# Kernel tuning notes

Hardware: AMD Instinct MI355X
Metric: run time of the kernel (lower is better)

Reference implementation:

```python
import jax, jax.numpy as jnp
import numpy as np
import math

H = 12          # num_attention_heads
DH = 64         # attention_head_size
LN_EPS = 1e-5


def layer_norm(x, gamma, beta):
    mu = jnp.mean(x, axis=-1, keepdims=True)
    var = jnp.mean(jnp.square(x - mu), axis=-1, keepdims=True)
    return (x - mu) * jax.lax.rsqrt(var + LN_EPS) * gamma + beta


def setup_inputs() -> dict:
    key = jax.random.key(0)
    ks = jax.random.split(key, 12)
    B, Lq, Lk, D = 4, 512, 512, 768
    s = 1.0 / math.sqrt(D)
    return {
        "hidden_states": jax.random.normal(ks[0], (B, Lq, D), jnp.float32),
        "context": jax.random.normal(ks[1], (B, Lk, D), jnp.float32),
        "attention_mask": jnp.zeros((B, 1, 1, Lk), jnp.float32),
        "graph_arc": jax.random.randint(ks[2], (B, Lq, Lk), 0, 3, jnp.int32),
        "Wq": jax.random.normal(ks[3], (D, D), jnp.float32) * s,
        "bq": jnp.zeros((D,), jnp.float32),
        "Wk": jax.random.normal(ks[4], (D, D), jnp.float32) * s,
        "bk": jnp.zeros((D,), jnp.float32),
        "Wv": jax.random.normal(ks[5], (D, D), jnp.float32) * s,
        "bv": jnp.zeros((D,), jnp.float32),
        "dpk_emb": jax.random.normal(ks[6], (3, DH), jnp.float32),
        "dpv_emb": jax.random.normal(ks[7], (3, DH), jnp.float32),
        "lnk_g": jnp.ones((DH,), jnp.float32),
        "lnk_b": jnp.zeros((DH,), jnp.float32),
        "lnv_g": jnp.ones((DH,), jnp.float32),
        "lnv_b": jnp.zeros((DH,), jnp.float32),
    }


def reference(hidden_states, context, attention_mask, graph_arc,
              Wq, bq, Wk, bk, Wv, bv,
              dpk_emb, dpv_emb, lnk_g, lnk_b, lnv_g, lnv_b):
    B, Lq, D = hidden_states.shape
    Lk = context.shape[1]

    def heads(x, L):  # [B,L,D] -> [B,H,L,dh]
        return x.reshape(B, L, H, DH).transpose(0, 2, 1, 3)

    q = heads(hidden_states @ Wq + bq, Lq)
    k = heads(context @ Wk + bk, Lk)
    v = heads(context @ Wv + bv, Lk)

    # relation embeddings per (query, key) pair: [B,Lq,Lk,dh]
    dp_keys = layer_norm(dpk_emb[graph_arc], lnk_g, lnk_b)
    dp_values = layer_norm(dpv_emb[graph_arc], lnv_g, lnv_b)

    scores = jnp.einsum('bhqd,bhkd->bhqk', q, k) / math.sqrt(DH)
    scores = scores + jnp.einsum('bhqd,bqkd->bhqk', q, dp_keys)
    scores = scores + attention_mask
    probs = jax.nn.softmax(scores, axis=-1)  # dropout p=0.0 -> identity

    ctx = jnp.einsum('bhqk,bhkd->bhqd', probs, v)
    ctx = ctx + jnp.einsum('bhqk,bqkd->bhqd', probs, dp_values)
    ctx = ctx.transpose(0, 2, 1, 3).reshape(B, Lq, D)
    return ctx
```

## Files before the change

kernel.cpp:

```cpp
#include <hip/hip_runtime.h>
#include <hip/hip_fp16.h>

#define NB 4
#define NH 12
#define DHD 64
#define LQ 512
#define LK 512
#define DM 768

typedef __attribute__((ext_vector_type(4))) _Float16 f16x4;
typedef __attribute__((ext_vector_type(8))) _Float16 f16x8;
typedef __attribute__((ext_vector_type(4))) float f32x4;

typedef __attribute__((address_space(1))) const unsigned int ga_uint;
typedef __attribute__((address_space(3))) unsigned int lds_uint;
__device__ static inline void gload_lds16(const void* g, void* l) {
    __builtin_amdgcn_global_load_lds((ga_uint*)g, (lds_uint*)l, 16, 0, 0);
}

__global__ __launch_bounds__(256) void prep_kernel(
    const float* __restrict__ Wq, const float* __restrict__ Wk,
    const float* __restrict__ Wv,
    const float* __restrict__ dpk, const float* __restrict__ dpv,
    const float* __restrict__ gk, const float* __restrict__ bk,
    const float* __restrict__ gv, const float* __restrict__ bv,
    _Float16* __restrict__ WT, float* __restrict__ lnK, float* __restrict__ lnV)
{
    const int bid = blockIdx.x, t = threadIdx.x;
    if (bid < 432) {
        __shared__ float sT[64][65];
        int mat = bid / 144, tile = bid % 144;
        int k0 = (tile / 12) * 64, n0 = (tile % 12) * 64;
        const float* W = (mat == 0) ? Wq : (mat == 1) ? Wk : Wv;
        #pragma unroll
        for (int p = 0; p < 4; ++p) {
            int idx = t + p * 256;
            int ki = idx >> 4, nj = (idx & 15) * 4;
            float4 wv = *(const float4*)&W[(size_t)(k0 + ki) * DM + n0 + nj];
            sT[ki][nj + 0] = wv.x; sT[ki][nj + 1] = wv.y;
            sT[ki][nj + 2] = wv.z; sT[ki][nj + 3] = wv.w;
        }
        __syncthreads();
        _Float16* dst = WT + (size_t)mat * DM * DM;
        #pragma unroll
        for (int p = 0; p < 4; ++p) {
            int idx = t + p * 256;
            int nr = idx >> 4, kj = (idx & 15) * 4;
            f16x4 hv = { (_Float16)sT[kj + 0][nr], (_Float16)sT[kj + 1][nr],
                         (_Float16)sT[kj + 2][nr], (_Float16)sT[kj + 3][nr] };
            *(f16x4*)&dst[(size_t)(n0 + nr) * DM + k0 + kj] = hv;
        }
    } else if (t < 64) {
        int lane = t;
        for (int r = 0; r < 3; ++r) {
            {
                float x = dpk[r * DHD + lane];
                float s = x;
                #pragma unroll
                for (int o = 1; o < 64; o <<= 1) s += __shfl_xor(s, o);
                float mu = s * (1.0f / 64.0f);
                float d = x - mu;
                float v = d * d;
                #pragma unroll
                for (int o = 1; o < 64; o <<= 1) v += __shfl_xor(v, o);
                lnK[r * DHD + lane] =
                    (d * rsqrtf(v * (1.0f / 64.0f) + 1e-5f) * gk[lane] + bk[lane]) * 8.0f;
            }
            {
                float x = dpv[r * DHD + lane];
                float s = x;
                #pragma unroll
                for (int o = 1; o < 64; o <<= 1) s += __shfl_xor(s, o);
                float mu = s * (1.0f / 64.0f);
                float d = x - mu;
                float v = d * d;
                #pragma unroll
                for (int o = 1; o < 64; o <<= 1) v += __shfl_xor(v, o);
                lnV[r * DHD + lane] =
                    d * rsqrtf(v * (1.0f / 64.0f) + 1e-5f) * gv[lane] + bv[lane];
            }
        }
    }
}

__global__ __launch_bounds__(256) void qkv_mfma(
    const float* __restrict__ hidden, const float* __restrict__ context,
    const _Float16* __restrict__ WT,
    const float* __restrict__ bq, const float* __restrict__ bk,
    const float* __restrict__ bv,
    _Float16* __restrict__ Qh, _Float16* __restrict__ Kh,
    _Float16* __restrict__ VTh)
{
    __shared__ __align__(16) char smem[21504];
    _Float16 (*sA)[72]  = (_Float16(*)[72])smem;
    char* sB            = smem + 9216;
    _Float16 (*sC)[104] = (_Float16(*)[104])smem;
    _Float16 (*sCV)[72] = (_Float16(*)[72])smem;

    const int t = threadIdx.x;
    const int w = t >> 6, lane = t & 63, g = lane >> 4, c16 = lane & 15;
    const int wm = w >> 1, wn = w & 1;
    const int mat = blockIdx.y / 8, nt0 = blockIdx.y % 8;
    const int m0 = blockIdx.x * 64, n0 = nt0 * 96;
    const float* X     = (mat == 0) ? hidden : context;
    const _Float16* Wt = WT + (size_t)mat * DM * DM;
    const float* bias  = (mat == 0) ? bq : (mat == 1) ? bk : bv;

    const int srow = (lane >> 3);
    const int sunit = (lane & 7) ^ srow;

    f32x4 acc[2][3];
    #pragma unroll
    for (int mt = 0; mt < 2; ++mt)
        #pragma unroll
        for (int nt = 0; nt < 3; ++nt) acc[mt][nt] = (f32x4){0.f, 0.f, 0.f, 0.f};

    for (int kt = 0; kt < 12; ++kt) {
        __syncthreads();
        #pragma unroll
        for (int p = 0; p < 4; ++p) {
            int idx = t + p * 256;
            int row = idx >> 4, c4 = idx & 15;
            float4 xv = *(const float4*)&X[(size_t)(m0 + row) * DM + kt * 64 + c4 * 4];
            f16x4 hv = { (_Float16)xv.x, (_Float16)xv.y,
                         (_Float16)xv.z, (_Float16)xv.w };
            *(f16x4*)&sA[row][c4 * 4] = hv;
        }
        #pragma unroll
        for (int cc = 0; cc < 3; ++cc) {
            int chunk = w * 3 + cc;
            int row = chunk * 8 + srow;
            gload_lds16(
                (const char*)&Wt[(size_t)(n0 + row) * DM + kt * 64] + sunit * 16,
                sB + chunk * 1024);
        }
        __syncthreads();
        #pragma unroll
        for (int kh = 0; kh < 2; ++kh) {
            f16x8 af[2], bf[3];
            #pragma unroll
            for (int mt = 0; mt < 2; ++mt)
                af[mt] = *(const f16x8*)&sA[wm * 32 + mt * 16 + c16][kh * 32 + 8 * g];
            #pragma unroll
            for (int nt = 0; nt < 3; ++nt) {
                int rn = wn * 48 + nt * 16 + c16;
                int boff = (rn * 128 + kh * 64 + g * 16) ^ ((rn & 7) << 4);
                bf[nt] = *(const f16x8*)(sB + boff);
            }
            #pragma unroll
            for (int mt = 0; mt < 2; ++mt)
                #pragma unroll
                for (int nt = 0; nt < 3; ++nt)
                    acc[mt][nt] = __builtin_amdgcn_mfma_f32_16x16x32_f16(
                        af[mt], bf[nt], acc[mt][nt], 0, 0, 0);
        }
    }

    const float sc = (mat == 0) ? 0.125f : 1.0f;
    float bb[3];
    #pragma unroll
    for (int nt = 0; nt < 3; ++nt)
        bb[nt] = bias[n0 + wn * 48 + nt * 16 + c16] * sc;
    __syncthreads();

    const int bbat = m0 >> 9, l0 = m0 & 511;
    if (mat < 2) {
        #pragma unroll
        for (int mt = 0; mt < 2; ++mt)
            #pragma unroll
            for (int nt = 0; nt < 3; ++nt)
                #pragma unroll
                for (int r = 0; r < 4; ++r)
                    sC[wm * 32 + mt * 16 + 4 * g + r][wn * 48 + nt * 16 + c16] =
                        (_Float16)(acc[mt][nt][r] * sc + bb[nt]);
        __syncthreads();
        _Float16* dst = (mat == 0) ? Qh : Kh;
        int row = t >> 2, qc = t & 3;
        #pragma unroll
        for (int j = 0; j < 3; ++j) {
            int col = qc * 24 + j * 8;
            int hd = (n0 + col) >> 6, d8 = (n0 + col) & 63;
            *(f16x8*)&dst[((size_t)(bbat * NH + hd) * LQ + l0 + row) * DHD + d8] =
                *(const f16x8*)&sC[row][col];
        }
    } else {
        #pragma unroll
        for (int mt = 0; mt < 2; ++mt)
            #pragma unroll
            for (int nt = 0; nt < 3; ++nt)
                #pragma unroll
                for (int r = 0; r < 4; ++r)
                    sCV[wn * 48 + nt * 16 + c16][wm * 32 + mt * 16 + 4 * g + r] =
                        (_Float16)(acc[mt][nt][r] + bb[nt]);
        __syncthreads();
        #pragma unroll
        for (int p = 0; p < 3; ++p) {
            int idx = t + p * 256;
            int n = idx >> 3, c8 = idx & 7;
            *(f16x8*)&VTh[((size_t)(bbat * NH + ((n0 + n) >> 6)) * DHD + ((n0 + n) & 63)) * LK
                          + l0 + c8 * 8] = *(const f16x8*)&sCV[n][c8 * 8];
        }
    }
}

__global__ __launch_bounds__(256) void attn_mfma(
    const _Float16* __restrict__ Qh, const _Float16* __restrict__ Kh,
    const _Float16* __restrict__ VTh, const float* __restrict__ maskp,
    const int* __restrict__ garc, const float* __restrict__ lnK,
    const float* __restrict__ lnV, float* __restrict__ outp)
{
    __shared__ __align__(16) _Float16 sP[32][520];
    __shared__ unsigned int sArcW[32 * 33];
    __shared__ float sTb[32][4];
    __shared__ float sMax[4][32];
    __shared__ float sStat[4][32][4];
    __shared__ float sFin[32][4];

    const int t = threadIdx.x;
    const int w = t >> 6, lane = t & 63, g = lane >> 4, c16 = lane & 15;
    const int bx = blockIdx.x;
    const int qt = bx & 15, h = (bx >> 4) % NH, b = bx / (16 * NH);
    const int q0 = qt * 32;
    const int kw = w * 128;

    const _Float16* Qb = Qh + ((size_t)(b * NH + h) * LQ) * DHD;
    const _Float16* Kb = Kh + ((size_t)(b * NH + h) * LK) * DHD;
    const _Float16* Vb = VTh + ((size_t)(b * NH + h) * DHD) * LK;

    const int* garcRow = garc + ((size_t)(b * LQ + q0)) * LK;
    #pragma unroll
    for (int p = 0; p < 4; ++p) {
        int idx = t + p * 256;
        int row = idx >> 5, wd = idx & 31;
        const int4* src = (const int4*)&garcRow[idx * 16];
        unsigned int u = 0;
        #pragma unroll
        for (int j = 0; j < 4; ++j) {
            int4 a4 = src[j];
            u |= (unsigned int)a4.x << (j * 8 + 0);
            u |= (unsigned int)a4.y << (j * 8 + 2);
            u |= (unsigned int)a4.z << (j * 8 + 4);
            u |= (unsigned int)a4.w << (j * 8 + 6);
        }
        sArcW[row * 33 + wd] = u;
    }
    if (t < 192) {
        int q = t / 6, rem = t % 6, rr = rem >> 1, part = rem & 1;
        const _Float16* qp = Qb + (size_t)(q0 + q) * DHD + part * 32;
        const float* lp = lnK + rr * 64 + part * 32;
        float a = 0.f;
        #pragma unroll
        for (int j = 0; j < 4; ++j) {
            f16x8 qv = *(const f16x8*)&qp[j * 8];
            float4 l0 = *(const float4*)&lp[j * 8];
            float4 l1 = *(const float4*)&lp[j * 8 + 4];
            a += (float)qv[0] * l0.x + (float)qv[1] * l0.y
               + (float)qv[2] * l0.z + (float)qv[3] * l0.w
               + (float)qv[4] * l1.x + (float)qv[5] * l1.y
               + (float)qv[6] * l1.z + (float)qv[7] * l1.w;
        }
        a += __shfl_xor(a, 1);
        if (part == 0) sTb[q][rr] = a;
    }
    f16x8 qa[2][2];
    #pragma unroll
    for (int qg = 0; qg < 2; ++qg) {
        qa[qg][0] = *(const f16x8*)&Qb[(q0 + 16 * qg + c16) * DHD + 8 * g];
        qa[qg][1] = *(const f16x8*)&Qb[(q0 + 16 * qg + c16) * DHD + 32 + 8 * g];
    }
    __syncthreads();

    f32x4 c[8][2];
    unsigned int aPk[2][2] = {{0u, 0u}, {0u, 0u}};
    float rm[2][4];
    const int sh = c16 * 2;
    #pragma unroll
    for (int qg = 0; qg < 2; ++qg)
        #pragma unroll
        for (int r = 0; r < 4; ++r) rm[qg][r] = -1e30f;
    #pragma unroll
    for (int tt = 0; tt < 8; ++tt) {
        int kg = kw + tt * 16 + c16;
        f16x8 kb0 = *(const f16x8*)&Kb[kg * DHD + 8 * g];
        f16x8 kb1 = *(const f16x8*)&Kb[kg * DHD + 32 + 8 * g];
        float mv = maskp[b * LK + kg];
        const int wb = w * 8 + tt;
        #pragma unroll
        for (int qg = 0; qg < 2; ++qg) {
            f32x4 s = (f32x4){0.f, 0.f, 0.f, 0.f};
            s = __builtin_amdgcn_mfma_f32_16x16x32_f16(qa[qg][0], kb0, s, 0, 0, 0);
            s = __builtin_amdgcn_mfma_f32_16x16x32_f16(qa[qg][1], kb1, s, 0, 0, 0);
            #pragma unroll
            for (int r = 0; r < 4; ++r) {
                int qrow = 16 * qg + 4 * g + r;
                unsigned int a = (sArcW[qrow * 33 + wb] >> sh) & 3u;
                aPk[qg][tt >> 2] |= a << ((tt & 3) * 8 + 2 * r);
                float sv = s[r] + sTb[qrow][a] + mv;
                s[r] = sv;
                rm[qg][r] = fmaxf(rm[qg][r], sv);
            }
            c[tt][qg] = s;
        }
    }

    #pragma unroll
    for (int qg = 0; qg < 2; ++qg)
        #pragma unroll
        for (int r = 0; r < 4; ++r) {
            float m = rm[qg][r];
            m = fmaxf(m, __shfl_xor(m, 1));
            m = fmaxf(m, __shfl_xor(m, 2));
            m = fmaxf(m, __shfl_xor(m, 4));
            m = fmaxf(m, __shfl_xor(m, 8));
            rm[qg][r] = m;
        }
    if (c16 == 0)
        #pragma unroll
        for (int qg = 0; qg < 2; ++qg)
            #pragma unroll
            for (int r = 0; r < 4; ++r) sMax[w][16 * qg + 4 * g + r] = rm[qg][r];
    __syncthreads();
    float Mr[2][4];
    #pragma unroll
    for (int qg = 0; qg < 2; ++qg)
        #pragma unroll
        for (int r = 0; r < 4; ++r) {
            int q = 16 * qg + 4 * g + r;
            Mr[qg][r] = fmaxf(fmaxf(sMax[0][q], sMax[1][q]),
                              fmaxf(sMax[2][q], sMax[3][q]));
        }

    float b0s[2][4], b1s[2][4], b2s[2][4];
    #pragma unroll
    for (int qg = 0; qg < 2; ++qg)
        #pragma unroll
        for (int r = 0; r < 4; ++r) {
            b0s[qg][r] = 0.f; b1s[qg][r] = 0.f; b2s[qg][r] = 0.f;
        }
    #pragma unroll
    for (int tt = 0; tt < 8; ++tt) {
        int kg = kw + tt * 16 + c16;
        #pragma unroll
        for (int qg = 0; qg < 2; ++qg)
            #pragma unroll
            for (int r = 0; r < 4; ++r) {
                float e = __expf(c[tt][qg][r] - Mr[qg][r]);
                unsigned int a = (aPk[qg][tt >> 2] >> ((tt & 3) * 8 + 2 * r)) & 3u;
                b0s[qg][r] += (a == 0u) ? e : 0.f;
                b1s[qg][r] += (a == 1u) ? e : 0.f;
                b2s[qg][r] += (a == 2u) ? e : 0.f;
                sP[16 * qg + 4 * g + r][kg] = (_Float16)e;
            }
    }
    #pragma unroll
    for (int qg = 0; qg < 2; ++qg)
        #pragma unroll
        for (int r = 0; r < 4; ++r) {
            #pragma unroll
            for (int o = 1; o < 16; o <<= 1) {
                b0s[qg][r] += __shfl_xor(b0s[qg][r], o);
                b1s[qg][r] += __shfl_xor(b1s[qg][r], o);
                b2s[qg][r] += __shfl_xor(b2s[qg][r], o);
            }
        }
    if (c16 == 0)
        #pragma unroll
        for (int qg = 0; qg < 2; ++qg)
            #pragma unroll
            for (int r = 0; r < 4; ++r) {
                float4 v = make_float4(b0s[qg][r], b1s[qg][r], b2s[qg][r], 0.f);
                *(float4*)&sStat[w][16 * qg + 4 * g + r][0] = v;
            }
    __syncthreads();
    if (t < 32) {
        float4 tot = make_float4(0.f, 0.f, 0.f, 0.f);
        #pragma unroll
        for (int ww = 0; ww < 4; ++ww) {
            float4 v = *(const float4*)&sStat[ww][t][0];
            tot.x += v.x; tot.y += v.y; tot.z += v.z;
        }
        sFin[t][0] = 1.0f / (tot.x + tot.y + tot.z);
        sFin[t][1] = tot.x; sFin[t][2] = tot.y; sFin[t][3] = tot.z;
    }

    f32x4 o[2] = {(f32x4){0.f, 0.f, 0.f, 0.f}, (f32x4){0.f, 0.f, 0.f, 0.f}};
    const _Float16* vrow = Vb + (size_t)(w * 16 + c16) * LK;
    #pragma unroll
    for (int ktile = 0; ktile < 16; ++ktile) {
        f16x8 vb = *(const f16x8*)&vrow[ktile * 32 + 8 * g];
        #pragma unroll
        for (int qg = 0; qg < 2; ++qg) {
            f16x8 pa = *(const f16x8*)&sP[16 * qg + c16][ktile * 32 + 8 * g];
            o[qg] = __builtin_amdgcn_mfma_f32_16x16x32_f16(pa, vb, o[qg], 0, 0, 0);
        }
    }
    __syncthreads();

    int d = w * 16 + c16;
    float lv0 = lnV[d], lv1 = lnV[64 + d], lv2 = lnV[128 + d];
    #pragma unroll
    for (int qg = 0; qg < 2; ++qg)
        #pragma unroll
        for (int r = 0; r < 4; ++r) {
            int q = 16 * qg + 4 * g + r;
            float4 st = *(const float4*)&sFin[q][0];
            float val = (o[qg][r] + st.y * lv0 + st.z * lv1 + st.w * lv2) * st.x;
            outp[((size_t)(b * LQ + q0 + q)) * DM + h * DHD + d] = val;
        }
}

extern "C" void kernel_launch(void* const* d_in, const int* in_sizes, int n_in,
                              void* d_out, int out_size, void* d_ws, size_t ws_size,
                              hipStream_t stream) {
    const float* hidden  = (const float*)d_in[0];
    const float* context = (const float*)d_in[1];
    const float* mask    = (const float*)d_in[2];
    const int*   garc    = (const int*)d_in[3];
    const float* Wq = (const float*)d_in[4];
    const float* bq = (const float*)d_in[5];
    const float* Wk = (const float*)d_in[6];
    const float* bk = (const float*)d_in[7];
    const float* Wv = (const float*)d_in[8];
    const float* bv = (const float*)d_in[9];
    const float* dpk  = (const float*)d_in[10];
    const float* dpv  = (const float*)d_in[11];
    const float* lnkg = (const float*)d_in[12];
    const float* lnkb = (const float*)d_in[13];
    const float* lnvg = (const float*)d_in[14];
    const float* lnvb = (const float*)d_in[15];
    float* out = (float*)d_out;

    const size_t perT = (size_t)NB * NH * LQ * DHD;
    _Float16* Qh  = (_Float16*)d_ws;
    _Float16* Kh  = Qh + perT;
    _Float16* VTh = Kh + perT;
    _Float16* WT  = VTh + perT;
    float* lnK = (float*)(WT + (size_t)3 * DM * DM);
    float* lnV = lnK + 192;

    prep_kernel<<<433, 256, 0, stream>>>(Wq, Wk, Wv, dpk, dpv,
                                         lnkg, lnkb, lnvg, lnvb, WT, lnK, lnV);
    qkv_mfma<<<dim3(32, 24), 256, 0, stream>>>(hidden, context, WT,
                                               bq, bk, bv, Qh, Kh, VTh);
    attn_mfma<<<768, 256, 0, stream>>>(Qh, Kh, VTh, mask, garc, lnK, lnV, out);
}
```

Measured before the change: 139.7 us.

## Double-buffer QKV projection GEMM tiles to overlap global loads with MFMA

Restructures the QKV projection k-loop to use double-buffered LDS for both the activation tile and the weight tile. The next tile's activations are loaded into registers and its weights are fetched async into the other buffer while MFMAs run on the current buffer, cutting one barrier per iteration. This doubles LDS use to about 42KB, which may reduce occupancy, and adds register pressure from holding the prefetched float4 values.

```diff
diff --git a/kernel.cpp b/kernel.cpp
--- a/kernel.cpp
+++ b/kernel.cpp
@@ -91,9 +91,8 @@
     _Float16* __restrict__ Qh, _Float16* __restrict__ Kh,
     _Float16* __restrict__ VTh)
 {
-    __shared__ __align__(16) char smem[21504];
-    _Float16 (*sA)[72]  = (_Float16(*)[72])smem;
-    char* sB            = smem + 9216;
+    __shared__ __align__(16) char smem[43008];
+    _Float16 (*sA)[64][72] = (_Float16(*)[64][72])smem;
     _Float16 (*sC)[104] = (_Float16(*)[104])smem;
     _Float16 (*sCV)[72] = (_Float16(*)[72])smem;
 
@@ -106,9 +105,27 @@
     const _Float16* Wt = WT + (size_t)mat * DM * DM;
     const float* bias  = (mat == 0) ? bq : (mat == 1) ? bk : bv;
 
-    const int srow = (lane >> 3);
+    const int srow  = lane >> 3;
     const int sunit = (lane & 7) ^ srow;
 
+    #pragma unroll
+    for (int p = 0; p < 4; ++p) {
+        int idx = t + p * 256;
+        int row = idx >> 4, c4 = idx & 15;
+        float4 xv = *(const float4*)&X[(size_t)(m0 + row) * DM + c4 * 4];
+        f16x4 hv = { (_Float16)xv.x, (_Float16)xv.y,
+                     (_Float16)xv.z, (_Float16)xv.w };
+        *(f16x4*)&sA[0][row][c4 * 4] = hv;
+    }
+    #pragma unroll
+    for (int cc = 0; cc < 3; ++cc) {
+        int chunk = w * 3 + cc;
+        int row = chunk * 8 + srow;
+        gload_lds16((const char*)&Wt[(size_t)(n0 + row) * DM] + sunit * 16,
+                    smem + 18432 + chunk * 1024);
+    }
+    __syncthreads();
+
     f32x4 acc[2][3];
     #pragma unroll
     for (int mt = 0; mt < 2; ++mt)
@@ -116,36 +133,37 @@
         for (int nt = 0; nt < 3; ++nt) acc[mt][nt] = (f32x4){0.f, 0.f, 0.f, 0.f};
 
     for (int kt = 0; kt < 12; ++kt) {
-        __syncthreads();
-        #pragma unroll
-        for (int p = 0; p < 4; ++p) {
-            int idx = t + p * 256;
-            int row = idx >> 4, c4 = idx & 15;
-            float4 xv = *(const float4*)&X[(size_t)(m0 + row) * DM + kt * 64 + c4 * 4];
-            f16x4 hv = { (_Float16)xv.x, (_Float16)xv.y,
-                         (_Float16)xv.z, (_Float16)xv.w };
-            *(f16x4*)&sA[row][c4 * 4] = hv;
-        }
-        #pragma unroll
-        for (int cc = 0; cc < 3; ++cc) {
-            int chunk = w * 3 + cc;
-            int row = chunk * 8 + srow;
-            gload_lds16(
-                (const char*)&Wt[(size_t)(n0 + row) * DM + kt * 64] + sunit * 16,
-                sB + chunk * 1024);
-        }
-        __syncthreads();
+        const int cur = kt & 1, nxt = cur ^ 1;
+        char* sBc = smem + 18432 + cur * 12288;
+        char* sBn = smem + 18432 + nxt * 12288;
+        float4 xv[4];
+        if (kt < 11) {
+            #pragma unroll
+            for (int p = 0; p < 4; ++p) {
+                int idx = t + p * 256;
+                int row = idx >> 4, c4 = idx & 15;
+                xv[p] = *(const float4*)&X[(size_t)(m0 + row) * DM + (kt + 1) * 64 + c4 * 4];
+            }
+            #pragma unroll
+            for (int cc = 0; cc < 3; ++cc) {
+                int chunk = w * 3 + cc;
+                int row = chunk * 8 + srow;
+                gload_lds16(
+                    (const char*)&Wt[(size_t)(n0 + row) * DM + (kt + 1) * 64] + sunit * 16,
+                    sBn + chunk * 1024);
+            }
+        }
         #pragma unroll
         for (int kh = 0; kh < 2; ++kh) {
             f16x8 af[2], bf[3];
             #pragma unroll
             for (int mt = 0; mt < 2; ++mt)
-                af[mt] = *(const f16x8*)&sA[wm * 32 + mt * 16 + c16][kh * 32 + 8 * g];
+                af[mt] = *(const f16x8*)&sA[cur][wm * 32 + mt * 16 + c16][kh * 32 + 8 * g];
             #pragma unroll
             for (int nt = 0; nt < 3; ++nt) {
                 int rn = wn * 48 + nt * 16 + c16;
                 int boff = (rn * 128 + kh * 64 + g * 16) ^ ((rn & 7) << 4);
-                bf[nt] = *(const f16x8*)(sB + boff);
+                bf[nt] = *(const f16x8*)(sBc + boff);
             }
             #pragma unroll
             for (int mt = 0; mt < 2; ++mt)
@@ -154,6 +172,17 @@
                     acc[mt][nt] = __builtin_amdgcn_mfma_f32_16x16x32_f16(
                         af[mt], bf[nt], acc[mt][nt], 0, 0, 0);
         }
+        if (kt < 11) {
+            #pragma unroll
+            for (int p = 0; p < 4; ++p) {
+                int idx = t + p * 256;
+                int row = idx >> 4, c4 = idx & 15;
+                f16x4 hv = { (_Float16)xv[p].x, (_Float16)xv[p].y,
+                             (_Float16)xv[p].z, (_Float16)xv[p].w };
+                *(f16x4*)&sA[nxt][row][c4 * 4] = hv;
+            }
+        }
+        __syncthreads();
     }
 
     const float sc = (mat == 0) ? 0.125f : 1.0f;
```

After: 138.3 us. No clear change (-1.0%).
